# Kernel optimization log

Hardware: AMD Instinct MI355X
Metric: run time of the kernel (lower is better)

## Reference

```python
import jax, jax.numpy as jnp
import numpy as np

N = 16384
F = 256
RATIO = 0.5
K_KEEP = int(RATIO * N)  # 8192 nodes kept


def setup_inputs() -> dict:
    key = jax.random.key(0)
    k1, k2, k3 = jax.random.split(key, 3)
    X = jax.random.normal(k1, (N, F), dtype=jnp.float32)
    # binary-ish dense adjacency
    A = (jax.random.uniform(k2, (N, N), dtype=jnp.float32) < 0.01).astype(jnp.float32)
    p = jax.random.normal(k3, (F, 1), dtype=jnp.float32)
    return {"X": X, "A": A, "p": p}


def reference(X, A, p):
    # y = X p / ||p||  (scores), shape [N, 1]
    p_hat = p / jnp.sqrt(jnp.sum(p * p))
    y = X @ p_hat
    # global top-k (single-graph mode: I == zeros), indices sorted ascending
    _, idx = jax.lax.top_k(y[:, 0], K_KEEP)
    idx = jnp.sort(idx)
    # gated features, then gather kept nodes
    features = X * jnp.tanh(y)
    X_pooled = jnp.take(features, idx, axis=0)          # [K, F]
    # adjacency submatrix A[idx, idx]
    A_pooled = jnp.take(jnp.take(A, idx, axis=0), idx, axis=1)  # [K, K]
    return X_pooled, A_pooled
```

## Files before the change

### kernel.cpp

```cpp
#include <hip/hip_runtime.h>
#include <math.h>

#define N 16384
#define F 256
#define K_KEEP 8192
#define QS 4096
#define APOOL_BLOCKS (K_KEEP * 4)

typedef float f32x4 __attribute__((ext_vector_type(4)));

__global__ __launch_bounds__(256) void score_kernel(const float* __restrict__ X,
                                                    const float* __restrict__ p,
                                                    float* __restrict__ y) {
    const int wave = threadIdx.x >> 6;
    const int lane = threadIdx.x & 63;
    const int row  = blockIdx.x * 4 + wave;

    const float4 pv = *reinterpret_cast<const float4*>(p + lane * 4);
    const float4 xv = *reinterpret_cast<const float4*>(X + (size_t)row * F + lane * 4);

    double pp = (double)pv.x * pv.x + (double)pv.y * pv.y +
                (double)pv.z * pv.z + (double)pv.w * pv.w;
    double xp = (double)xv.x * pv.x + (double)xv.y * pv.y +
                (double)xv.z * pv.z + (double)xv.w * pv.w;

    #pragma unroll
    for (int off = 32; off >= 1; off >>= 1) {
        pp += __shfl_down(pp, off, 64);
        xp += __shfl_down(xp, off, 64);
    }
    if (lane == 0) y[row] = (float)(xp / sqrt(pp));
}

__global__ __launch_bounds__(256) void select_emit_kernel(const float* __restrict__ y,
                                                          int* __restrict__ idx,
                                                          unsigned short* __restrict__ srcq,
                                                          int* __restrict__ wexcl) {
    __shared__ int hist[4096];
    __shared__ int part[256];
    __shared__ int sc[256];
    __shared__ int bres[2];
    __shared__ float cand[1024];
    __shared__ int ccnt;
    __shared__ float sthr;
    __shared__ unsigned long long fbw[256];
    const int t = threadIdx.x;

    #pragma unroll
    for (int q = 0; q < 16; ++q) hist[q * 256 + t] = 0;
    if (t == 0) ccnt = 0;
    __syncthreads();

    for (int i = t; i < N; i += 256) {
        const float v = fminf(fmaxf(y[i] * 341.3333f + 2048.0f, 0.0f), 4095.0f);
        atomicAdd(&hist[(int)v], 1);
    }
    __syncthreads();

    int ps = 0;
    #pragma unroll
    for (int q = 0; q < 16; ++q) ps += hist[t * 16 + q];
    part[t] = ps;
    __syncthreads();
    for (int off = 1; off < 256; off <<= 1) {
        const int v = (t >= off) ? part[t - off] : 0;
        __syncthreads();
        part[t] += v;
        __syncthreads();
    }
    int acc = part[255] - part[t];
    int fbin = -1, fr = 0;
    #pragma unroll
    for (int q = 15; q >= 0; --q) {
        const int b = t * 16 + q;
        const int h = hist[b];
        if (fbin < 0 && acc <= K_KEEP - 1 && K_KEEP - 1 < acc + h) {
            fbin = b; fr = K_KEEP - acc;
        }
        acc += h;
    }
    if (fbin >= 0) { bres[0] = fbin; bres[1] = fr; }
    __syncthreads();
    const int bstar = bres[0];
    const int r     = bres[1];

    for (int i = t; i < N; i += 256) {
        const float yv = y[i];
        const float v = fminf(fmaxf(yv * 341.3333f + 2048.0f, 0.0f), 4095.0f);
        if ((int)v == bstar) {
            const int pos = atomicAdd(&ccnt, 1);
            if (pos < 1024) cand[pos] = yv;
        }
    }
    __syncthreads();
    const int cc = (ccnt < 1024) ? ccnt : 1024;
    if (t < cc) {
        const float kk = cand[t];
        int g = 0;
        for (int j = 0; j < cc; ++j) g += (int)(cand[j] > kk);
        if (g == r - 1) sthr = kk;
    }
    __syncthreads();
    const float thr = sthr;

    const int wave = t >> 6;
    const int lane = t & 63;
    for (int q = 0; q < 64; ++q) {
        const bool kept = y[q * 256 + t] >= thr;
        const unsigned long long m = __ballot(kept);
        if (lane == 0) fbw[q * 4 + wave] = m;
    }
    __syncthreads();

    const unsigned long long m = fbw[t];
    const int c = __popcll(m);
    sc[t] = c;
    __syncthreads();
    for (int off = 1; off < 256; off <<= 1) {
        const int v = (t >= off) ? sc[t - off] : 0;
        __syncthreads();
        sc[t] += v;
        __syncthreads();
    }
    int base = sc[t] - c;
    wexcl[t] = base;
    unsigned long long mm = m;
    const int col = t * 64;
    while (mm) {
        const int b = __ffsll((long long)mm) - 1;
        mm &= (mm - 1);
        const int i = col + b;
        idx[base]  = i;
        srcq[base] = (unsigned short)(i & (QS - 1));
        ++base;
    }
}

__global__ __launch_bounds__(256) void pool_kernel(const float* __restrict__ A,
                                                   const float* __restrict__ X,
                                                   const float* __restrict__ y,
                                                   const int* __restrict__ idx,
                                                   const unsigned short* __restrict__ srcq,
                                                   const int* __restrict__ wexcl,
                                                   float* __restrict__ outX,
                                                   float* __restrict__ outA) {
    const int t = threadIdx.x;

    if (blockIdx.x >= APOOL_BLOCKS) {
        const int k    = (blockIdx.x - APOOL_BLOCKS) * 4 + (t >> 6);
        const int lane = t & 63;
        const int src  = idx[k];
        const float tf = tanhf(y[src]);
        const float4 xv = *reinterpret_cast<const float4*>(X + (size_t)src * F + lane * 4);
        float4 o = {xv.x * tf, xv.y * tf, xv.z * tf, xv.w * tf};
        *reinterpret_cast<float4*>(outX + (size_t)k * F + lane * 4) = o;
        return;
    }

    __shared__ float buf[QS];
    const int row  = blockIdx.x >> 2;
    const int h    = blockIdx.x & 3;
    const int ridx = idx[row];
    const int kb   = wexcl[h * 64];
    const int ke   = (h < 3) ? wexcl[h * 64 + 64] : K_KEEP;

    const f32x4* __restrict__ a4 =
        reinterpret_cast<const f32x4*>(A + (size_t)ridx * N + h * QS);
    f32x4* __restrict__ b4 = reinterpret_cast<f32x4*>(buf);
    #pragma unroll
    for (int s = 0; s < 4; ++s) b4[s * 256 + t] = __builtin_nontemporal_load(a4 + s * 256 + t);
    __syncthreads();

    float* __restrict__ orow = outA + (size_t)row * K_KEEP;
    const int k4b = (kb + 3) & ~3;
    const int k4e = ke & ~3;
    if (t < (k4b - kb)) orow[kb + t] = buf[srcq[kb + t]];
    if (t < (ke - k4e)) orow[k4e + t] = buf[srcq[k4e + t]];
    for (int k4 = k4b + 4 * t; k4 < k4e; k4 += 1024) {
        const ushort4 s4 = *reinterpret_cast<const ushort4*>(srcq + k4);
        f32x4 v = {buf[s4.x], buf[s4.y], buf[s4.z], buf[s4.w]};
        __builtin_nontemporal_store(v, reinterpret_cast<f32x4*>(orow + k4));
    }
}

extern "C" void kernel_launch(void* const* d_in, const int* in_sizes, int n_in,
                              void* d_out, int out_size, void* d_ws, size_t ws_size,
                              hipStream_t stream) {
    const float* X = (const float*)d_in[0];
    const float* A = (const float*)d_in[1];
    const float* p = (const float*)d_in[2];

    float* out  = (float*)d_out;
    float* outX = out;
    float* outA = out + (size_t)K_KEEP * F;

    char* ws = (char*)d_ws;
    float*          y     = (float*)ws;
    int*            wexcl = (int*)(ws + 65536);
    int*            idx   = (int*)(ws + 66560);
    unsigned short* srcq  = (unsigned short*)(ws + 99328);

    score_kernel<<<N / 4, 256, 0, stream>>>(X, p, y);
    select_emit_kernel<<<1, 256, 0, stream>>>(y, idx, srcq, wexcl);
    pool_kernel<<<APOOL_BLOCKS + K_KEEP / 4, 256, 0, stream>>>(A, X, y, idx, srcq, wexcl,
                                                               outX, outA);
}
```

Baseline: 190.6 us.

## Widen single-block top-k select to 1024 threads and keep scores in registers

The single-block selection kernel now runs with 1024 threads instead of 256. Each thread loads its 16 contiguous scores once with vector loads and keeps them and their bin indices in registers. The histogram, candidate and mask passes reuse those values instead of rereading global memory three times. Per-thread keep masks are built locally as 16-bit words and packed into 64-bit words for the existing 256-thread scan and emit, which adds a longer 1024-entry prefix scan and some idle threads during emit.

```diff
diff --git a/kernel.cpp b/kernel.cpp
--- a/kernel.cpp
+++ b/kernel.cpp
@@ -32,47 +32,55 @@
     if (lane == 0) y[row] = (float)(xp / sqrt(pp));
 }
 
-__global__ __launch_bounds__(256) void select_emit_kernel(const float* __restrict__ y,
-                                                          int* __restrict__ idx,
-                                                          unsigned short* __restrict__ srcq,
-                                                          int* __restrict__ wexcl) {
+__global__ __launch_bounds__(1024) void select_emit_kernel(const float* __restrict__ y,
+                                                           int* __restrict__ idx,
+                                                           unsigned short* __restrict__ srcq,
+                                                           int* __restrict__ wexcl) {
     __shared__ int hist[4096];
-    __shared__ int part[256];
+    __shared__ int part[1024];
     __shared__ int sc[256];
     __shared__ int bres[2];
     __shared__ float cand[1024];
     __shared__ int ccnt;
     __shared__ float sthr;
-    __shared__ unsigned long long fbw[256];
+    __shared__ unsigned short fbw16[1024];
     const int t = threadIdx.x;
 
     #pragma unroll
-    for (int q = 0; q < 16; ++q) hist[q * 256 + t] = 0;
+    for (int q = 0; q < 4; ++q) hist[q * 1024 + t] = 0;
     if (t == 0) ccnt = 0;
     __syncthreads();
 
-    for (int i = t; i < N; i += 256) {
-        const float v = fminf(fmaxf(y[i] * 341.3333f + 2048.0f, 0.0f), 4095.0f);
-        atomicAdd(&hist[(int)v], 1);
-    }
-    __syncthreads();
-
-    int ps = 0;
-    #pragma unroll
-    for (int q = 0; q < 16; ++q) ps += hist[t * 16 + q];
-    part[t] = ps;
-    __syncthreads();
-    for (int off = 1; off < 256; off <<= 1) {
+    float yv[16];
+    const float4* __restrict__ y4 = reinterpret_cast<const float4*>(y + t * 16);
+    #pragma unroll
+    for (int q = 0; q < 4; ++q) {
+        const float4 v = y4[q];
+        yv[q * 4 + 0] = v.x; yv[q * 4 + 1] = v.y;
+        yv[q * 4 + 2] = v.z; yv[q * 4 + 3] = v.w;
+    }
+    int bins[16];
+    #pragma unroll
+    for (int j = 0; j < 16; ++j) {
+        const float v = fminf(fmaxf(yv[j] * 341.3333f + 2048.0f, 0.0f), 4095.0f);
+        bins[j] = (int)v;
+        atomicAdd(&hist[bins[j]], 1);
+    }
+    __syncthreads();
+
+    part[t] = hist[t * 4] + hist[t * 4 + 1] + hist[t * 4 + 2] + hist[t * 4 + 3];
+    __syncthreads();
+    for (int off = 1; off < 1024; off <<= 1) {
         const int v = (t >= off) ? part[t - off] : 0;
         __syncthreads();
         part[t] += v;
         __syncthreads();
     }
-    int acc = part[255] - part[t];
+    int acc = part[1023] - part[t];
     int fbin = -1, fr = 0;
     #pragma unroll
-    for (int q = 15; q >= 0; --q) {
-        const int b = t * 16 + q;
+    for (int q = 3; q >= 0; --q) {
+        const int b = t * 4 + q;
         const int h = hist[b];
         if (fbin < 0 && acc <= K_KEEP - 1 && K_KEEP - 1 < acc + h) {
             fbin = b; fr = K_KEEP - acc;
@@ -84,12 +92,11 @@
     const int bstar = bres[0];
     const int r     = bres[1];
 
-    for (int i = t; i < N; i += 256) {
-        const float yv = y[i];
-        const float v = fminf(fmaxf(yv * 341.3333f + 2048.0f, 0.0f), 4095.0f);
-        if ((int)v == bstar) {
+    #pragma unroll
+    for (int j = 0; j < 16; ++j) {
+        if (bins[j] == bstar) {
             const int pos = atomicAdd(&ccnt, 1);
-            if (pos < 1024) cand[pos] = yv;
+            if (pos < 1024) cand[pos] = yv[j];
         }
     }
     __syncthreads();
@@ -103,36 +110,41 @@
     __syncthreads();
     const float thr = sthr;
 
-    const int wave = t >> 6;
-    const int lane = t & 63;
-    for (int q = 0; q < 64; ++q) {
-        const bool kept = y[q * 256 + t] >= thr;
-        const unsigned long long m = __ballot(kept);
-        if (lane == 0) fbw[q * 4 + wave] = m;
-    }
-    __syncthreads();
-
-    const unsigned long long m = fbw[t];
-    const int c = __popcll(m);
-    sc[t] = c;
+    unsigned int mask = 0;
+    #pragma unroll
+    for (int j = 0; j < 16; ++j) mask |= ((unsigned int)(yv[j] >= thr)) << j;
+    fbw16[t] = (unsigned short)mask;
+    __syncthreads();
+
+    unsigned long long m = 0;
+    if (t < 256) {
+        m = (unsigned long long)fbw16[4 * t]
+          | ((unsigned long long)fbw16[4 * t + 1] << 16)
+          | ((unsigned long long)fbw16[4 * t + 2] << 32)
+          | ((unsigned long long)fbw16[4 * t + 3] << 48);
+        sc[t] = __popcll(m);
+    }
     __syncthreads();
     for (int off = 1; off < 256; off <<= 1) {
-        const int v = (t >= off) ? sc[t - off] : 0;
-        __syncthreads();
-        sc[t] += v;
-        __syncthreads();
-    }
-    int base = sc[t] - c;
-    wexcl[t] = base;
-    unsigned long long mm = m;
-    const int col = t * 64;
-    while (mm) {
-        const int b = __ffsll((long long)mm) - 1;
-        mm &= (mm - 1);
-        const int i = col + b;
-        idx[base]  = i;
-        srcq[base] = (unsigned short)(i & (QS - 1));
-        ++base;
+        const int v = (t >= off && t < 256) ? sc[t - off] : 0;
+        __syncthreads();
+        if (t < 256) sc[t] += v;
+        __syncthreads();
+    }
+    if (t < 256) {
+        const int c = __popcll(m);
+        int base = sc[t] - c;
+        wexcl[t] = base;
+        unsigned long long mm = m;
+        const int col = t * 64;
+        while (mm) {
+            const int b = __ffsll((long long)mm) - 1;
+            mm &= (mm - 1);
+            const int i = col + b;
+            idx[base]  = i;
+            srcq[base] = (unsigned short)(i & (QS - 1));
+            ++base;
+        }
     }
 }
 
@@ -201,7 +213,7 @@
     unsigned short* srcq  = (unsigned short*)(ws + 99328);
 
     score_kernel<<<N / 4, 256, 0, stream>>>(X, p, y);
-    select_emit_kernel<<<1, 256, 0, stream>>>(y, idx, srcq, wexcl);
+    select_emit_kernel<<<1, 1024, 0, stream>>>(y, idx, srcq, wexcl);
     pool_kernel<<<APOOL_BLOCKS + K_KEEP / 4, 256, 0, stream>>>(A, X, y, idx, srcq, wexcl,
                                                                outX, outA);
 }
```

After: 160.7 us (median of 2 runs). -15.7%, faster.
